# Optimization experiments

Measured on AMD Instinct MI355X. Metric: run time of the kernel, lower is better.

Reference implementation:

```python
import jax, jax.numpy as jnp
import numpy as np

N_NODES = 50000
N_EDGES = 400000


def gat(x, src, dst, W, al, ar, b, n):
    # DGL GATConv: fc -> per-head attention logits -> edge softmax over dst -> weighted sum
    heads, dout = al.shape
    z = (x.reshape(-1, x.shape[-1]) @ W.T).reshape(n, heads, dout)   # [N,H,D]
    el = jnp.sum(z * al, axis=-1)                                    # [N,H]
    er = jnp.sum(z * ar, axis=-1)                                    # [N,H]
    e = jax.nn.leaky_relu(el[src] + er[dst], negative_slope=0.2)     # [E,H]
    emax = jax.ops.segment_max(e, dst, num_segments=n)               # [N,H]
    emax = jnp.where(jnp.isfinite(emax), emax, 0.0)                  # zero-in-degree nodes
    ee = jnp.exp(e - emax[dst])
    den = jax.ops.segment_sum(ee, dst, num_segments=n)               # [N,H]
    alpha = ee / den[dst]                                            # edge softmax
    rst = jax.ops.segment_sum(alpha[:, :, None] * z[src], dst, num_segments=n)  # [N,H,D]
    return rst + b.reshape(heads, dout)


def chain_pass(h, src, dst, n):
    # constrainLayer: m_e = z_src - z_dst, sum at dst, then L2-normalize last dim
    m = jax.ops.segment_sum(h[src] - h[dst], dst, num_segments=n)
    l = jnp.sqrt(jnp.sum(m * m, axis=-1, keepdims=True)) + 1e-7
    return m / l


def setup_inputs() -> dict:
    key = jax.random.key(0)
    ks = jax.random.split(key, 32)
    n, e = N_NODES, N_EDGES
    in_dim, hid, out, H = 64, 128, 64, 4

    def nrm(k, shape, s=0.05):
        return jax.random.normal(k, shape, dtype=jnp.float32) * s

    inp = {
        "x": nrm(ks[0], (n, in_dim), 1.0),
        "src0": jax.random.randint(ks[1], (e,), 0, n, dtype=jnp.int32),
        "dst0": jax.random.randint(ks[2], (e,), 0, n, dtype=jnp.int32),
        "src1": jnp.arange(n - 1, dtype=jnp.int32),
        "dst1": jnp.arange(1, n, dtype=jnp.int32),
        # layer1 (in->hid, 1 head) per etype
        "W1a": nrm(ks[3], (hid, in_dim)), "al1a": nrm(ks[4], (1, hid)), "ar1a": nrm(ks[5], (1, hid)), "b1a": nrm(ks[6], (hid,)),
        "W1b": nrm(ks[7], (hid, in_dim)), "al1b": nrm(ks[8], (1, hid)), "ar1b": nrm(ks[9], (1, hid)), "b1b": nrm(ks[10], (hid,)),
        # layer2 (hid->out, 1 head) per etype
        "W2a": nrm(ks[11], (out, hid)), "al2a": nrm(ks[12], (1, out)), "ar2a": nrm(ks[13], (1, out)), "b2a": nrm(ks[14], (out,)),
        "W2b": nrm(ks[15], (out, hid)), "al2b": nrm(ks[16], (1, out)), "ar2b": nrm(ks[17], (1, out)), "b2b": nrm(ks[18], (out,)),
        # layerMH (out->out, H heads) per etype
        "Wma": nrm(ks[19], (H * out, out)), "alma": nrm(ks[20], (H, out)), "arma": nrm(ks[21], (H, out)), "bma": nrm(ks[22], (H * out,)),
        "Wmb": nrm(ks[23], (H * out, out)), "almb": nrm(ks[24], (H, out)), "armb": nrm(ks[25], (H, out)), "bmb": nrm(ks[26], (H * out,)),
        "r": jax.random.uniform(ks[27], (1,), dtype=jnp.float32),
    }
    return inp


def reference(x, src0, dst0, src1, dst1,
              W1a, al1a, ar1a, b1a, W1b, al1b, ar1b, b1b,
              W2a, al2a, ar2a, b2a, W2b, al2b, ar2b, b2b,
              Wma, alma, arma, bma, Wmb, almb, armb, bmb, r):
    n = x.shape[0]
    # HeteroGraphConv(mean) over etypes {interacts, chain}
    h = 0.5 * (gat(x, src0, dst0, W1a, al1a, ar1a, b1a, n)
               + gat(x, src1, dst1, W1b, al1b, ar1b, b1b, n))          # [N,1,hid]
    h = 0.5 * (gat(h, src0, dst0, W2a, al2a, ar2a, b2a, n)
               + gat(h, src1, dst1, W2b, al2b, ar2b, b2b, n))          # [N,1,out]
    radius = jnp.clip(r, 0.01, 3.0)  # computed but unused (dead code in original)
    dh = chain_pass(h, src1, dst1, n)                                   # [N,1,out]
    conh = jnp.cumsum(dh, axis=-2)  # cumsum over singleton head axis (as in original)
    hm = 0.5 * (gat(conh, src0, dst0, Wma, alma, arma, bma, n)
                + gat(conh, src1, dst1, Wmb, almb, armb, bmb, n))       # [N,H,out]
    # per-head chain pass + cumsum over nodes, vectorized across heads
    ds = chain_pass(hm, src1, dst1, n)                                  # [N,H,out]
    res = jnp.cumsum(ds, axis=0)                                        # torch cumsum dim=-2 of [N,out] per head
    return res
```

## Files before the change

### kernel.cpp

```cpp
#include <hip/hip_runtime.h>
#include <math.h>

__device__ __forceinline__ float wred_sum(float v){
  #pragma unroll
  for (int o = 32; o > 0; o >>= 1) v += __shfl_xor(v, o);
  return v;
}
__device__ __forceinline__ float wred_max(float v){
  #pragma unroll
  for (int o = 32; o > 0; o >>= 1) v = fmaxf(v, __shfl_xor(v, o));
  return v;
}
__device__ __forceinline__ float lrelu(float v){ return v > 0.f ? v : 0.2f * v; }
__device__ __forceinline__ float sel4(int h, float4 v){
  return (h & 2) ? ((h & 1) ? v.w : v.z) : ((h & 1) ? v.y : v.x);
}

__global__ void k_hist(const int* __restrict__ dst, int* __restrict__ deg, int E){
  int t = blockIdx.x * blockDim.x + threadIdx.x;
  if (t < E) atomicAdd(&deg[dst[t]], 1);
}

__global__ void k_deg_bsum(const int* __restrict__ deg, int* __restrict__ bsum, int n){
  __shared__ int s[256];
  int b = blockIdx.x, t = threadIdx.x;
  int i = b * 256 + t;
  s[t] = (i < n) ? deg[i] : 0;
  __syncthreads();
  for (int o = 128; o > 0; o >>= 1){ if (t < o) s[t] += s[t + o]; __syncthreads(); }
  if (t == 0) bsum[b] = s[0];
}
__global__ void k_bsum_scan(int* __restrict__ bsum, int nblk){
  __shared__ int s[256];
  int t = threadIdx.x;
  s[t] = (t < nblk) ? bsum[t] : 0;
  __syncthreads();
  for (int o = 1; o < 256; o <<= 1){
    int add = (t >= o) ? s[t - o] : 0;
    __syncthreads();
    s[t] += add;
    __syncthreads();
  }
  if (t < nblk) bsum[t] = (t > 0) ? s[t - 1] : 0;
}
__global__ void k_rowptr(const int* __restrict__ deg, const int* __restrict__ bsum,
                         int* __restrict__ rowptr, int* __restrict__ cursor, int n, int E){
  __shared__ int s[256];
  int b = blockIdx.x, t = threadIdx.x;
  int i = b * 256 + t;
  int v = (i < n) ? deg[i] : 0;
  s[t] = v;
  __syncthreads();
  for (int o = 1; o < 256; o <<= 1){
    int add = (t >= o) ? s[t - o] : 0;
    __syncthreads();
    s[t] += add;
    __syncthreads();
  }
  if (i < n){
    int rp = bsum[b] + s[t] - v;
    rowptr[i] = rp;
    cursor[i] = rp;
    if (i == n - 1) rowptr[n] = E;
  }
}

__global__ void k_scatter(const int* __restrict__ src, const int* __restrict__ dst,
                          int* __restrict__ cursor, int* __restrict__ esrc, int E){
  int t = blockIdx.x * blockDim.x + threadIdx.x;
  if (t < E){
    int d = dst[t];
    int p = atomicAdd(&cursor[d], 1);
    esrc[p] = src[t];
  }
}

__global__ void k_valvar_all(const float* __restrict__ W1, const float* __restrict__ al1, const float* __restrict__ ar1,
                             const float* __restrict__ W2, const float* __restrict__ al2, const float* __restrict__ ar2,
                             const float* __restrict__ Wm, const float* __restrict__ alm, const float* __restrict__ arm,
                             float* __restrict__ vv1, float* __restrict__ vv2, float* __restrict__ vvm){
  int b = blockIdx.x, k = threadIdx.x;
  if (b == 0){
    if (k < 64){
      float v = 0.f, w = 0.f;
      for (int c = 0; c < 128; c++){ float ww = W1[c * 64 + k]; v += al1[c] * ww; w += ar1[c] * ww; }
      vv1[k] = v; vv1[64 + k] = w;
    }
  } else if (b == 1){
    float v = 0.f, w = 0.f;
    for (int c = 0; c < 64; c++){ float ww = W2[c * 128 + k]; v += al2[c] * ww; w += ar2[c] * ww; }
    vv2[k] = v; vv2[128 + k] = w;
  } else {
    if (k < 64){
      for (int h = 0; h < 4; h++){
        float v = 0.f, w = 0.f;
        for (int c = 0; c < 64; c++){
          float ww = Wm[(size_t)(h * 64 + c) * 64 + k];
          v += alm[h * 64 + c] * ww; w += arm[h * 64 + c] * ww;
        }
        vvm[(2 * h) * 64 + k] = v; vvm[(2 * h + 1) * 64 + k] = w;
      }
    }
  }
}

template<int K, int C, int H>
__global__ void k_gemm2(const float* __restrict__ x,
                        const float* __restrict__ Wa, const float* __restrict__ Wb,
                        const float* __restrict__ vv,
                        float* __restrict__ za, float* __restrict__ zb,
                        float* __restrict__ el, float* __restrict__ er, int n){
  constexpr int K4 = K / 4, NKC = K / 64, NCC = C / 64;
  constexpr int ROWS = 16384 / (K * 4);
  constexpr int RPW = ROWS / 4;
  constexpr int NP = NCC;
  __shared__ float  XS[ROWS][K];
  __shared__ float4 WQ[2][16 * 65];

  int t = threadIdx.x, lane = t & 63, wv = t >> 6;
  int rowbase = blockIdx.x * ROWS;

  for (int idx = t; idx < ROWS * K4; idx += 256){
    int r = idx / K4, k4 = idx - r * K4;
    int row = rowbase + r;
    float4 v = make_float4(0.f, 0.f, 0.f, 0.f);
    if (row < n) v = *(const float4*)&x[(size_t)row * K + k4 * 4];
    *(float4*)&XS[r][k4 * 4] = v;
  }

  const int r0 = wv * RPW;
  float acc0[RPW], acc1[RPW];

  for (int p = 0; p < NP; p++){
    int q0 = 2 * p, q1 = q0 + 1;
    const float* Wp0 = (q0 < NCC) ? (Wa + (size_t)q0 * 64 * K) : (Wb + (size_t)(q0 - NCC) * 64 * K);
    const float* Wp1 = (q1 < NCC) ? (Wa + (size_t)q1 * 64 * K) : (Wb + (size_t)(q1 - NCC) * 64 * K);
    #pragma unroll
    for (int r = 0; r < RPW; r++){ acc0[r] = 0.f; acc1[r] = 0.f; }

    for (int kc = 0; kc < NKC; kc++){
      __syncthreads();
      const float4* A4 = (const float4*)Wp0;
      const float4* B4 = (const float4*)Wp1;
      for (int idx = t; idx < 1024; idx += 256){
        int c = idx >> 4, k4 = idx & 15;
        WQ[0][k4 * 65 + c] = A4[(size_t)c * K4 + kc * 16 + k4];
        WQ[1][k4 * 65 + c] = B4[(size_t)c * K4 + kc * 16 + k4];
      }
      __syncthreads();
      #pragma unroll 4
      for (int k4 = 0; k4 < 16; k4++){
        float4 w0 = WQ[0][k4 * 65 + lane];
        float4 w1 = WQ[1][k4 * 65 + lane];
        #pragma unroll
        for (int r = 0; r < RPW; r++){
          float4 xk = *(const float4*)&XS[r0 + r][kc * 64 + k4 * 4];
          acc0[r] += xk.x * w0.x + xk.y * w0.y + xk.z * w0.z + xk.w * w0.w;
          acc1[r] += xk.x * w1.x + xk.y * w1.y + xk.z * w1.z + xk.w * w1.w;
        }
      }
    }

    float* z0 = (q0 < NCC) ? za : zb;
    float* z1 = (q1 < NCC) ? za : zb;
    int c0 = ((q0 < NCC) ? q0 : q0 - NCC) * 64;
    int c1 = ((q1 < NCC) ? q1 : q1 - NCC) * 64;
    #pragma unroll
    for (int r = 0; r < RPW; r++){
      int row = rowbase + r0 + r;
      if (row < n){
        z0[(size_t)row * C + c0 + lane] = acc0[r];
        z1[(size_t)row * C + c1 + lane] = acc1[r];
      }
    }
  }

  {
    #pragma unroll
    for (int r = 0; r < RPW; r++) acc0[r] = 0.f;
    for (int kc = 0; kc < NKC; kc++){
      __syncthreads();
      const float4* V4 = (const float4*)vv;
      for (int idx = t; idx < 2 * H * 16; idx += 256){
        int c = idx >> 4, k4 = idx & 15;
        WQ[0][k4 * 65 + c] = V4[(size_t)c * K4 + kc * 16 + k4];
      }
      __syncthreads();
      #pragma unroll 4
      for (int k4 = 0; k4 < 16; k4++){
        float4 w0 = WQ[0][k4 * 65 + lane];
        #pragma unroll
        for (int r = 0; r < RPW; r++){
          float4 xk = *(const float4*)&XS[r0 + r][kc * 64 + k4 * 4];
          acc0[r] += xk.x * w0.x + xk.y * w0.y + xk.z * w0.z + xk.w * w0.w;
        }
      }
    }
    if (lane < 2 * H){
      int h = lane >> 1;
      float* dst = (lane & 1) ? er : el;
      #pragma unroll
      for (int r = 0; r < RPW; r++){
        int row = rowbase + r0 + r;
        if (row < n) dst[(size_t)row * H + h] = acc0[r];
      }
    }
  }
}

template<int D>
__global__ void k_gat_h1(const int* __restrict__ rowptr, const int* __restrict__ esrc,
                         const float* __restrict__ z, const float* __restrict__ el,
                         const float* __restrict__ er, const float* __restrict__ b,
                         const float* __restrict__ zb, const float* __restrict__ bb,
                         float* __restrict__ out, int n){
  constexpr int LPS = D / 4;
  constexpr int NS  = 64 / LPS;
  int lane = threadIdx.x & 63;
  int q = lane / LPS, j = lane % LPS;
  int i = blockIdx.x * (blockDim.x >> 6) + (threadIdx.x >> 6);
  if (i >= n) return;
  int s0 = rowptr[i], s1 = rowptr[i + 1];
  float eri = er[i];
  float m = -INFINITY;
  for (int e = s0 + lane; e < s1; e += 64)
    m = fmaxf(m, lrelu(el[esrc[e]] + eri));
  m = wred_max(m);
  float4 acc = make_float4(0.f, 0.f, 0.f, 0.f);
  float den = 0.f;
  for (int base = s0; base < s1; base += NS){
    int e = base + q;
    bool ok = (e < s1);
    int s = esrc[ok ? e : s0];
    float w = ok ? __expf(lrelu(el[s] + eri) - m) : 0.f;
    den += w;
    float4 zv = *(const float4*)&z[(size_t)s * D + 4 * j];
    acc.x += w * zv.x; acc.y += w * zv.y; acc.z += w * zv.z; acc.w += w * zv.w;
  }
  #pragma unroll
  for (int o = LPS; o < 64; o <<= 1){
    acc.x += __shfl_xor(acc.x, o);
    acc.y += __shfl_xor(acc.y, o);
    acc.z += __shfl_xor(acc.z, o);
    acc.w += __shfl_xor(acc.w, o);
    den   += __shfl_xor(den, o);
  }
  float inv = (s1 > s0) ? 1.f / den : 0.f;
  if (lane < LPS){
    float4 bv  = *(const float4*)&b[4 * j];
    float4 ch  = *(const float4*)&bb[4 * j];
    if (i > 0){
      float4 zbv = *(const float4*)&zb[(size_t)(i - 1) * D + 4 * j];
      ch.x += zbv.x; ch.y += zbv.y; ch.z += zbv.z; ch.w += zbv.w;
    }
    float4 o4;
    o4.x = 0.5f * ((acc.x * inv + bv.x) + ch.x);
    o4.y = 0.5f * ((acc.y * inv + bv.y) + ch.y);
    o4.z = 0.5f * ((acc.z * inv + bv.z) + ch.z);
    o4.w = 0.5f * ((acc.w * inv + bv.w) + ch.w);
    *(float4*)&out[(size_t)i * D + 4 * j] = o4;
  }
}

__global__ void k_gat_mh(const int* __restrict__ rowptr, const int* __restrict__ esrc,
                         const float* __restrict__ z, const float* __restrict__ el,
                         const float* __restrict__ er, const float* __restrict__ b,
                         const float* __restrict__ zb, const float* __restrict__ bb,
                         float* __restrict__ out, int n){
  int lane = threadIdx.x & 63;
  int h = lane >> 4;
  int i = blockIdx.x * (blockDim.x >> 6) + (threadIdx.x >> 6);
  if (i >= n) return;
  int s0 = rowptr[i], s1 = rowptr[i + 1];
  const float4 eri4 = *(const float4*)(er + (size_t)i * 4);
  float m0 = -INFINITY, m1 = -INFINITY, m2 = -INFINITY, m3 = -INFINITY;
  for (int e = s0 + lane; e < s1; e += 64){
    float4 e4 = *(const float4*)(el + (size_t)esrc[e] * 4);
    m0 = fmaxf(m0, lrelu(e4.x + eri4.x));
    m1 = fmaxf(m1, lrelu(e4.y + eri4.y));
    m2 = fmaxf(m2, lrelu(e4.z + eri4.z));
    m3 = fmaxf(m3, lrelu(e4.w + eri4.w));
  }
  m0 = wred_max(m0); m1 = wred_max(m1); m2 = wred_max(m2); m3 = wred_max(m3);
  float msel = (h & 2) ? ((h & 1) ? m3 : m2) : ((h & 1) ? m1 : m0);
  float erh  = sel4(h, eri4);

  float4 acc  = make_float4(0.f, 0.f, 0.f, 0.f);
  float4 accB = make_float4(0.f, 0.f, 0.f, 0.f);
  float den = 0.f, denB = 0.f;
  int e = s0;
  for (; e + 1 < s1; e += 2){
    int sA = esrc[e], sB = esrc[e + 1];
    float4 eA = *(const float4*)(el + (size_t)sA * 4);
    float4 eB = *(const float4*)(el + (size_t)sB * 4);
    float wA = __expf(lrelu(sel4(h, eA) + erh) - msel);
    float wB = __expf(lrelu(sel4(h, eB) + erh) - msel);
    den += wA; denB += wB;
    float4 zA = *(const float4*)&z[(size_t)sA * 256 + 4 * lane];
    float4 zB = *(const float4*)&z[(size_t)sB * 256 + 4 * lane];
    acc.x  += wA * zA.x; acc.y  += wA * zA.y; acc.z  += wA * zA.z; acc.w  += wA * zA.w;
    accB.x += wB * zB.x; accB.y += wB * zB.y; accB.z += wB * zB.z; accB.w += wB * zB.w;
  }
  if (e < s1){
    int sA = esrc[e];
    float4 eA = *(const float4*)(el + (size_t)sA * 4);
    float wA = __expf(lrelu(sel4(h, eA) + erh) - msel);
    den += wA;
    float4 zA = *(const float4*)&z[(size_t)sA * 256 + 4 * lane];
    acc.x += wA * zA.x; acc.y += wA * zA.y; acc.z += wA * zA.z; acc.w += wA * zA.w;
  }
  den += denB;
  acc.x += accB.x; acc.y += accB.y; acc.z += accB.z; acc.w += accB.w;
  float inv = (s1 > s0) ? 1.f / den : 0.f;

  float4 bv = *(const float4*)&b[4 * lane];
  float4 ch = *(const float4*)&bb[4 * lane];
  if (i > 0){
    float4 zbv = *(const float4*)&zb[(size_t)(i - 1) * 256 + 4 * lane];
    ch.x += zbv.x; ch.y += zbv.y; ch.z += zbv.z; ch.w += zbv.w;
  }
  float4 o4;
  o4.x = 0.5f * ((acc.x * inv + bv.x) + ch.x);
  o4.y = 0.5f * ((acc.y * inv + bv.y) + ch.y);
  o4.z = 0.5f * ((acc.z * inv + bv.z) + ch.z);
  o4.w = 0.5f * ((acc.w * inv + bv.w) + ch.w);
  *(float4*)&out[(size_t)i * 256 + 4 * lane] = o4;
}

__global__ void k_chainpass64(const float* __restrict__ h, float* __restrict__ dh, int n){
  int lane = threadIdx.x & 63;
  int i = blockIdx.x * (blockDim.x >> 6) + (threadIdx.x >> 6);
  if (i >= n) return;
  float d = 0.f;
  if (i > 0) d = h[(size_t)(i - 1) * 64 + lane] - h[(size_t)i * 64 + lane];
  float ss = wred_sum(d * d);
  dh[(size_t)i * 64 + lane] = d / (sqrtf(ss) + 1e-7f);
}

__global__ void k_chainpass_mh(const float* __restrict__ hm, float* __restrict__ ds, int n){
  int lane = threadIdx.x & 63;
  int i = blockIdx.x * (blockDim.x >> 6) + (threadIdx.x >> 6);
  if (i >= n) return;
  const float* cur = hm + (size_t)i * 256;
  const float* prv = hm + (size_t)(i - 1) * 256;
  #pragma unroll
  for (int h = 0; h < 4; h++){
    int c = h * 64 + lane;
    float d = (i > 0) ? (prv[c] - cur[c]) : 0.f;
    float ss = wred_sum(d * d);
    ds[(size_t)i * 256 + c] = d / (sqrtf(ss) + 1e-7f);
  }
}

__global__ void k_chunk_sum(const float* __restrict__ ds, float* __restrict__ csum, int n, int ch){
  int b = blockIdx.x, t = threadIdx.x;
  int r0 = b * ch, r1 = r0 + ch; if (r1 > n) r1 = n;
  float s = 0.f;
  for (int r = r0; r < r1; r++) s += ds[(size_t)r * 256 + t];
  csum[(size_t)b * 256 + t] = s;
}
__global__ void k_scan_chunks_par(float* __restrict__ csum, int nb){
  __shared__ float s[512];
  int col = blockIdx.x;
  int t = threadIdx.x;
  s[t] = (t < nb) ? csum[(size_t)t * 256 + col] : 0.f;
  __syncthreads();
  #pragma unroll
  for (int o = 1; o < 512; o <<= 1){
    float add = (t >= o) ? s[t - o] : 0.f;
    __syncthreads();
    s[t] += add;
    __syncthreads();
  }
  if (t < nb) csum[(size_t)t * 256 + col] = (t > 0) ? s[t - 1] : 0.f;
}
__global__ void k_apply_scan(float* __restrict__ ds, const float* __restrict__ csum, int n, int ch){
  int b = blockIdx.x, t = threadIdx.x;
  int r0 = b * ch, r1 = r0 + ch; if (r1 > n) r1 = n;
  float run = csum[(size_t)b * 256 + t];
  for (int r = r0; r < r1; r++){
    run += ds[(size_t)r * 256 + t];
    ds[(size_t)r * 256 + t] = run;
  }
}

extern "C" void kernel_launch(void* const* d_in, const int* in_sizes, int n_in,
                              void* d_out, int out_size, void* d_ws, size_t ws_size,
                              hipStream_t stream){
  const float* x    = (const float*)d_in[0];
  const int*   src0 = (const int*)d_in[1];
  const int*   dst0 = (const int*)d_in[2];
  const float* W1a  = (const float*)d_in[5];
  const float* al1a = (const float*)d_in[6];
  const float* ar1a = (const float*)d_in[7];
  const float* b1a  = (const float*)d_in[8];
  const float* W1b  = (const float*)d_in[9];
  const float* b1b  = (const float*)d_in[12];
  const float* W2a  = (const float*)d_in[13];
  const float* al2a = (const float*)d_in[14];
  const float* ar2a = (const float*)d_in[15];
  const float* b2a  = (const float*)d_in[16];
  const float* W2b  = (const float*)d_in[17];
  const float* b2b  = (const float*)d_in[20];
  const float* Wma  = (const float*)d_in[21];
  const float* alma = (const float*)d_in[22];
  const float* arma = (const float*)d_in[23];
  const float* bma  = (const float*)d_in[24];
  const float* Wmb  = (const float*)d_in[25];
  const float* bmb  = (const float*)d_in[28];

  const int n = in_sizes[0] / 64;
  const int E = in_sizes[1];
  const size_t nf = (size_t)n;

  float* ws  = (float*)d_ws;
  float* A   = ws;
  float* B   = A + nf * 256;
  float* C   = B + nf * 256;
  float* D2  = C + nf * 256;
  float* E2  = D2 + nf * 64;
  float* ela = E2 + nf * 64;
  float* era = ela + nf * 4;
  const int ch = 100;
  const int nb = (n + ch - 1) / ch;
  float* csum = era + nf * 4;
  int* deg    = (int*)(csum + (size_t)nb * 256);
  int* rowptr = deg + n;
  int* cursor = rowptr + (n + 1);
  int* esrc   = cursor + n;
  int* bsum   = esrc + E;
  float* vv1  = (float*)(bsum + 256);
  float* vv2  = vv1 + 128;
  float* vvm  = vv2 + 256;

  float* dsout = (float*)d_out;

  const int nwb  = (n + 3) / 4;
  const int eb   = (E + 255) / 256;
  const int nblk = (n + 255) / 256;

  hipMemsetAsync(deg, 0, (size_t)n * sizeof(int), stream);
  k_hist<<<eb, 256, 0, stream>>>(dst0, deg, E);
  k_deg_bsum<<<nblk, 256, 0, stream>>>(deg, bsum, n);
  k_bsum_scan<<<1, 256, 0, stream>>>(bsum, nblk);
  k_rowptr<<<nblk, 256, 0, stream>>>(deg, bsum, rowptr, cursor, n, E);
  k_scatter<<<eb, 256, 0, stream>>>(src0, dst0, cursor, esrc, E);

  k_valvar_all<<<3, 128, 0, stream>>>(W1a, al1a, ar1a, W2a, al2a, ar2a, Wma, alma, arma,
                                      vv1, vv2, vvm);

  k_gemm2<64, 128, 1><<<(n + 63) / 64, 256, 0, stream>>>(x, W1a, W1b, vv1, A, B, ela, era, n);
  k_gat_h1<128><<<nwb, 256, 0, stream>>>(rowptr, esrc, A, ela, era, b1a, B, b1b, C, n);

  k_gemm2<128, 64, 1><<<(n + 31) / 32, 256, 0, stream>>>(C, W2a, W2b, vv2, A, B, ela, era, n);
  k_gat_h1<64><<<nwb, 256, 0, stream>>>(rowptr, esrc, A, ela, era, b2a, B, b2b, D2, n);

  k_chainpass64<<<nwb, 256, 0, stream>>>(D2, E2, n);

  k_gemm2<64, 256, 4><<<(n + 63) / 64, 256, 0, stream>>>(E2, Wma, Wmb, vvm, A, B, ela, era, n);
  k_gat_mh<<<nwb, 256, 0, stream>>>(rowptr, esrc, A, ela, era, bma, B, bmb, C, n);

  k_chainpass_mh<<<nwb, 256, 0, stream>>>(C, dsout, n);

  k_chunk_sum<<<nb, 256, 0, stream>>>(dsout, csum, n, ch);
  k_scan_chunks_par<<<256, 512, 0, stream>>>(csum, nb);
  k_apply_scan<<<nb, 256, 0, stream>>>(dsout, csum, n, ch);
}
```

Before: 692.2 us.

## Pre-transpose weights once and stream them from global memory in GEMM kernels

A new kernel transposes all six weight matrices into a k4-major float4 layout once per call, and the attention-vector projections are stored in a matching interleaved layout. The GEMM kernels no longer stage weight tiles through shared memory with two barriers per chunk. Each lane instead reads its coalesced float4 weight column directly from global memory or cache. This removes the LDS staging traffic and synchronisation and lets only the lanes that need them compute the el/er projections, at the cost of one extra small launch and reliance on L2 for weight reuse across blocks.

```diff
diff --git a/kernel.cpp b/kernel.cpp
--- a/kernel.cpp
+++ b/kernel.cpp
@@ -75,21 +75,43 @@
   }
 }
 
+__global__ void k_wtrans_all(const float* __restrict__ W1a, const float* __restrict__ W1b,
+                             const float* __restrict__ W2a, const float* __restrict__ W2b,
+                             const float* __restrict__ Wma, const float* __restrict__ Wmb,
+                             float4* __restrict__ T1a, float4* __restrict__ T1b,
+                             float4* __restrict__ T2a, float4* __restrict__ T2b,
+                             float4* __restrict__ Tma, float4* __restrict__ Tmb){
+  int idx = blockIdx.x * 256 + threadIdx.x;
+  const float* W; float4* T; int C, K4, off;
+  if      (idx <  2048){ W = W1a; T = T1a; C = 128; K4 = 16; off = idx; }
+  else if (idx <  4096){ W = W1b; T = T1b; C = 128; K4 = 16; off = idx - 2048; }
+  else if (idx <  6144){ W = W2a; T = T2a; C =  64; K4 = 32; off = idx - 4096; }
+  else if (idx <  8192){ W = W2b; T = T2b; C =  64; K4 = 32; off = idx - 6144; }
+  else if (idx < 12288){ W = Wma; T = Tma; C = 256; K4 = 16; off = idx - 8192; }
+  else if (idx < 16384){ W = Wmb; T = Tmb; C = 256; K4 = 16; off = idx - 12288; }
+  else return;
+  int c = off / K4, k4 = off - c * K4;
+  const float* p = &W[(size_t)c * (K4 * 4) + 4 * k4];
+  T[(size_t)k4 * C + c] = make_float4(p[0], p[1], p[2], p[3]);
+}
+
 __global__ void k_valvar_all(const float* __restrict__ W1, const float* __restrict__ al1, const float* __restrict__ ar1,
                              const float* __restrict__ W2, const float* __restrict__ al2, const float* __restrict__ ar2,
                              const float* __restrict__ Wm, const float* __restrict__ alm, const float* __restrict__ arm,
-                             float* __restrict__ vv1, float* __restrict__ vv2, float* __restrict__ vvm){
+                             float* __restrict__ vvT1, float* __restrict__ vvT2, float* __restrict__ vvTm){
   int b = blockIdx.x, k = threadIdx.x;
   if (b == 0){
     if (k < 64){
       float v = 0.f, w = 0.f;
       for (int c = 0; c < 128; c++){ float ww = W1[c * 64 + k]; v += al1[c] * ww; w += ar1[c] * ww; }
-      vv1[k] = v; vv1[64 + k] = w;
+      vvT1[((k >> 2) * 2 + 0) * 4 + (k & 3)] = v;
+      vvT1[((k >> 2) * 2 + 1) * 4 + (k & 3)] = w;
     }
   } else if (b == 1){
     float v = 0.f, w = 0.f;
     for (int c = 0; c < 64; c++){ float ww = W2[c * 128 + k]; v += al2[c] * ww; w += ar2[c] * ww; }
-    vv2[k] = v; vv2[128 + k] = w;
+    vvT2[((k >> 2) * 2 + 0) * 4 + (k & 3)] = v;
+    vvT2[((k >> 2) * 2 + 1) * 4 + (k & 3)] = w;
   } else {
     if (k < 64){
       for (int h = 0; h < 4; h++){
@@ -98,112 +120,83 @@
           float ww = Wm[(size_t)(h * 64 + c) * 64 + k];
           v += alm[h * 64 + c] * ww; w += arm[h * 64 + c] * ww;
         }
-        vvm[(2 * h) * 64 + k] = v; vvm[(2 * h + 1) * 64 + k] = w;
+        vvTm[((k >> 2) * 8 + 2 * h + 0) * 4 + (k & 3)] = v;
+        vvTm[((k >> 2) * 8 + 2 * h + 1) * 4 + (k & 3)] = w;
       }
     }
   }
 }
 
 template<int K, int C, int H>
-__global__ void k_gemm2(const float* __restrict__ x,
-                        const float* __restrict__ Wa, const float* __restrict__ Wb,
-                        const float* __restrict__ vv,
-                        float* __restrict__ za, float* __restrict__ zb,
-                        float* __restrict__ el, float* __restrict__ er, int n){
-  constexpr int K4 = K / 4, NKC = K / 64, NCC = C / 64;
+__global__ void k_gemm2t(const float* __restrict__ x,
+                         const float4* __restrict__ WTa, const float4* __restrict__ WTb,
+                         const float4* __restrict__ vvT,
+                         float* __restrict__ za, float* __restrict__ zb,
+                         float* __restrict__ el, float* __restrict__ er, int n){
+  constexpr int K4 = K / 4, NCC = C / 64;
   constexpr int ROWS = 16384 / (K * 4);
   constexpr int RPW = ROWS / 4;
-  constexpr int NP = NCC;
-  __shared__ float  XS[ROWS][K];
-  __shared__ float4 WQ[2][16 * 65];
+  __shared__ float XS[ROWS][K];
 
   int t = threadIdx.x, lane = t & 63, wv = t >> 6;
   int rowbase = blockIdx.x * ROWS;
 
+  const float4* x4 = (const float4*)x;
   for (int idx = t; idx < ROWS * K4; idx += 256){
     int r = idx / K4, k4 = idx - r * K4;
     int row = rowbase + r;
     float4 v = make_float4(0.f, 0.f, 0.f, 0.f);
-    if (row < n) v = *(const float4*)&x[(size_t)row * K + k4 * 4];
+    if (row < n) v = x4[(size_t)row * K4 + k4];
     *(float4*)&XS[r][k4 * 4] = v;
   }
+  __syncthreads();
 
   const int r0 = wv * RPW;
   float acc0[RPW], acc1[RPW];
 
-  for (int p = 0; p < NP; p++){
-    int q0 = 2 * p, q1 = q0 + 1;
-    const float* Wp0 = (q0 < NCC) ? (Wa + (size_t)q0 * 64 * K) : (Wb + (size_t)(q0 - NCC) * 64 * K);
-    const float* Wp1 = (q1 < NCC) ? (Wa + (size_t)q1 * 64 * K) : (Wb + (size_t)(q1 - NCC) * 64 * K);
+  for (int p = 0; p < NCC; p++){
     #pragma unroll
     for (int r = 0; r < RPW; r++){ acc0[r] = 0.f; acc1[r] = 0.f; }
-
-    for (int kc = 0; kc < NKC; kc++){
-      __syncthreads();
-      const float4* A4 = (const float4*)Wp0;
-      const float4* B4 = (const float4*)Wp1;
-      for (int idx = t; idx < 1024; idx += 256){
-        int c = idx >> 4, k4 = idx & 15;
-        WQ[0][k4 * 65 + c] = A4[(size_t)c * K4 + kc * 16 + k4];
-        WQ[1][k4 * 65 + c] = B4[(size_t)c * K4 + kc * 16 + k4];
+    const float4* Wa4 = WTa + (size_t)p * 64 + lane;
+    const float4* Wb4 = WTb + (size_t)p * 64 + lane;
+    #pragma unroll 2
+    for (int k4 = 0; k4 < K4; k4++){
+      float4 w0 = Wa4[(size_t)k4 * C];
+      float4 w1 = Wb4[(size_t)k4 * C];
+      #pragma unroll
+      for (int r = 0; r < RPW; r++){
+        float4 xk = *(const float4*)&XS[r0 + r][k4 * 4];
+        acc0[r] += xk.x * w0.x + xk.y * w0.y + xk.z * w0.z + xk.w * w0.w;
+        acc1[r] += xk.x * w1.x + xk.y * w1.y + xk.z * w1.z + xk.w * w1.w;
       }
-      __syncthreads();
-      #pragma unroll 4
-      for (int k4 = 0; k4 < 16; k4++){
-        float4 w0 = WQ[0][k4 * 65 + lane];
-        float4 w1 = WQ[1][k4 * 65 + lane];
-        #pragma unroll
-        for (int r = 0; r < RPW; r++){
-          float4 xk = *(const float4*)&XS[r0 + r][kc * 64 + k4 * 4];
-          acc0[r] += xk.x * w0.x + xk.y * w0.y + xk.z * w0.z + xk.w * w0.w;
-          acc1[r] += xk.x * w1.x + xk.y * w1.y + xk.z * w1.z + xk.w * w1.w;
-        }
-      }
-    }
-
-    float* z0 = (q0 < NCC) ? za : zb;
-    float* z1 = (q1 < NCC) ? za : zb;
-    int c0 = ((q0 < NCC) ? q0 : q0 - NCC) * 64;
-    int c1 = ((q1 < NCC) ? q1 : q1 - NCC) * 64;
+    }
     #pragma unroll
     for (int r = 0; r < RPW; r++){
       int row = rowbase + r0 + r;
       if (row < n){
-        z0[(size_t)row * C + c0 + lane] = acc0[r];
-        z1[(size_t)row * C + c1 + lane] = acc1[r];
+        za[(size_t)row * C + p * 64 + lane] = acc0[r];
+        zb[(size_t)row * C + p * 64 + lane] = acc1[r];
       }
     }
   }
 
-  {
+  if (lane < 2 * H){
     #pragma unroll
     for (int r = 0; r < RPW; r++) acc0[r] = 0.f;
-    for (int kc = 0; kc < NKC; kc++){
-      __syncthreads();
-      const float4* V4 = (const float4*)vv;
-      for (int idx = t; idx < 2 * H * 16; idx += 256){
-        int c = idx >> 4, k4 = idx & 15;
-        WQ[0][k4 * 65 + c] = V4[(size_t)c * K4 + kc * 16 + k4];
-      }
-      __syncthreads();
-      #pragma unroll 4
-      for (int k4 = 0; k4 < 16; k4++){
-        float4 w0 = WQ[0][k4 * 65 + lane];
-        #pragma unroll
-        for (int r = 0; r < RPW; r++){
-          float4 xk = *(const float4*)&XS[r0 + r][kc * 64 + k4 * 4];
-          acc0[r] += xk.x * w0.x + xk.y * w0.y + xk.z * w0.z + xk.w * w0.w;
-        }
-      }
-    }
-    if (lane < 2 * H){
-      int h = lane >> 1;
-      float* dst = (lane & 1) ? er : el;
+    for (int k4 = 0; k4 < K4; k4++){
+      float4 w0 = vvT[(size_t)k4 * (2 * H) + lane];
       #pragma unroll
       for (int r = 0; r < RPW; r++){
-        int row = rowbase + r0 + r;
-        if (row < n) dst[(size_t)row * H + h] = acc0[r];
+        float4 xk = *(const float4*)&XS[r0 + r][k4 * 4];
+        acc0[r] += xk.x * w0.x + xk.y * w0.y + xk.z * w0.z + xk.w * w0.w;
       }
+    }
+    int h = lane >> 1;
+    float* dst = (lane & 1) ? er : el;
+    #pragma unroll
+    for (int r = 0; r < RPW; r++){
+      int row = rowbase + r0 + r;
+      if (row < n) dst[(size_t)row * H + h] = acc0[r];
     }
   }
 }
@@ -424,14 +417,21 @@
   const int ch = 100;
   const int nb = (n + ch - 1) / ch;
   float* csum = era + nf * 4;
-  int* deg    = (int*)(csum + (size_t)nb * 256);
+  float* wtbase = csum + (size_t)nb * 256;
+  float4* T1a = (float4*)wtbase;
+  float4* T1b = T1a + 2048;
+  float4* T2a = T1b + 2048;
+  float4* T2b = T2a + 2048;
+  float4* Tma = T2b + 2048;
+  float4* Tmb = Tma + 4096;
+  float* vvT1 = (float*)(Tmb + 4096);
+  float* vvT2 = vvT1 + 128;
+  float* vvTm = vvT2 + 256;
+  int* deg    = (int*)(vvTm + 512);
   int* rowptr = deg + n;
-  int* cursor = rowptr + (n + 1);
+  int* cursor = rowptr + (n + 16);
   int* esrc   = cursor + n;
   int* bsum   = esrc + E;
-  float* vv1  = (float*)(bsum + 256);
-  float* vv2  = vv1 + 128;
-  float* vvm  = vv2 + 256;
 
   float* dsout = (float*)d_out;
 
@@ -446,18 +446,20 @@
   k_rowptr<<<nblk, 256, 0, stream>>>(deg, bsum, rowptr, cursor, n, E);
   k_scatter<<<eb, 256, 0, stream>>>(src0, dst0, cursor, esrc, E);
 
+  k_wtrans_all<<<64, 256, 0, stream>>>(W1a, W1b, W2a, W2b, Wma, Wmb,
+                                       T1a, T1b, T2a, T2b, Tma, Tmb);
   k_valvar_all<<<3, 128, 0, stream>>>(W1a, al1a, ar1a, W2a, al2a, ar2a, Wma, alma, arma,
-                                      vv1, vv2, vvm);
-
-  k_gemm2<64, 128, 1><<<(n + 63) / 64, 256, 0, stream>>>(x, W1a, W1b, vv1, A, B, ela, era, n);
+                                      vvT1, vvT2, vvTm);
+
+  k_gemm2t<64, 128, 1><<<(n + 63) / 64, 256, 0, stream>>>(x, T1a, T1b, (const float4*)vvT1, A, B, ela, era, n);
   k_gat_h1<128><<<nwb, 256, 0, stream>>>(rowptr, esrc, A, ela, era, b1a, B, b1b, C, n);
 
-  k_gemm2<128, 64, 1><<<(n + 31) / 32, 256, 0, stream>>>(C, W2a, W2b, vv2, A, B, ela, era, n);
+  k_gemm2t<128, 64, 1><<<(n + 31) / 32, 256, 0, stream>>>(C, T2a, T2b, (const float4*)vvT2, A, B, ela, era, n);
   k_gat_h1<64><<<nwb, 256, 0, stream>>>(rowptr, esrc, A, ela, era, b2a, B, b2b, D2, n);
 
   k_chainpass64<<<nwb, 256, 0, stream>>>(D2, E2, n);
 
-  k_gemm2<64, 256, 4><<<(n + 63) / 64, 256, 0, stream>>>(E2, Wma, Wmb, vvm, A, B, ela, era, n);
+  k_gemm2t<64, 256, 4><<<(n + 63) / 64, 256, 0, stream>>>(E2, Tma, Tmb, (const float4*)vvTm, A, B, ela, era, n);
   k_gat_mh<<<nwb, 256, 0, stream>>>(rowptr, esrc, A, ela, era, bma, B, bmb, C, n);
 
   k_chainpass_mh<<<nwb, 256, 0, stream>>>(C, dsout, n);
```

Measured after the change: 691.1 us. No clear change (-0.1%).
